# Optimization experiments

Hardware: AMD Instinct MI355X
Metric: run time of the kernel (lower is better)

## Reference

```python
import math
import jax, jax.numpy as jnp
from jax import lax
import numpy as np

WH, WW = 5, 9          # window_size
EH, EW = 3, 5          # expand_size = ((ws+1)//2)
NHEAD = 4
D = 512
PK, PS = 4, 4          # pool kernel / stride


def _valid_ind_rolled():
    m = np.ones((4, WH, WW), dtype=np.float32)
    m[0, :WH - EH, :WW - EW] = 0  # tl
    m[1, :WH - EH, EW:] = 0       # tr
    m[2, EH:, :WW - EW] = 0       # bl
    m[3, EH:, EW:] = 0            # br
    return np.nonzero(m.reshape(-1))[0]

VALID_IND = jnp.asarray(_valid_ind_rolled())  # (148,)


def _forward(x, masks, Wq, bq, Wk, bk, Wv, bv, Wp, bp, pool_w, pool_b):
    b, t, h, w, c = x.shape
    hd = c // NHEAD
    n_wh, n_ww = h // WH, w // WW
    n_win = n_wh * n_ww
    S = WH * WW  # tokens per window per frame (45)

    q = x @ Wq + bq
    k = x @ Wk + bk
    v = x @ Wv + bv

    def wp(a):  # window partition -> (b, n_win, nhead, t, S, hd)
        a = a.reshape(b, t, n_wh, WH, n_ww, WW, NHEAD, hd)
        a = a.transpose(0, 2, 4, 6, 1, 3, 5, 7)
        return a.reshape(b, n_win, NHEAD, t, S, hd)

    win_q, win_k, win_v = wp(q), wp(k), wp(v)

    # rolled (shifted) windows, gathered by the static valid-index buffer
    shifts = ((-EH, -EW), (-EH, EW), (EH, -EW), (EH, EW))
    roll_k = jnp.concatenate([wp(jnp.roll(k, s, axis=(2, 3))) for s in shifts], axis=4)[:, :, :, :, VALID_IND]
    roll_v = jnp.concatenate([wp(jnp.roll(v, s, axis=(2, 3))) for s in shifts], axis=4)[:, :, :, :, VALID_IND]

    # pooled global tokens via depthwise conv (kernel 4, stride 4)
    px = lax.conv_general_dilated(
        x.reshape(b * t, h, w, c), pool_w, (PS, PS), 'VALID',
        dimension_numbers=('NHWC', 'HWIO', 'NHWC'), feature_group_count=c) + pool_b
    ph, pw = px.shape[1], px.shape[2]
    P = ph * pw
    px = px.reshape(b, t, P, c)

    def pool_tok(a):  # (b,t,P,c) -> (b,1,nhead,t,P,hd)
        return a.reshape(b, t, P, NHEAD, hd).transpose(0, 3, 1, 2, 4)[:, None]

    pk = jnp.broadcast_to(pool_tok(px @ Wk + bk), (b, n_win, NHEAD, t, P, hd))
    pv = jnp.broadcast_to(pool_tok(px @ Wv + bv), (b, n_win, NHEAD, t, P, hd))

    win_k_full = jnp.concatenate([win_k, roll_k, pk], axis=4)  # (b,n_win,nh,t,K,hd)
    win_v_full = jnp.concatenate([win_v, roll_v, pv], axis=4)
    K = win_k_full.shape[4]

    # window-level mask: max-pool per window per frame, summed over frames, >0
    wmask = masks[..., 0].reshape(b, t, n_wh, WH, n_ww, WW).max(axis=(3, 5))
    wmask = wmask.reshape(b, t, n_win).sum(axis=1) > 0  # (b, n_win)

    scale = 1.0 / math.sqrt(hd)

    # dense spatiotemporal attention (used for masked windows)
    qd = win_q.reshape(b, n_win, NHEAD, t * S, hd)
    kd = win_k_full.reshape(b, n_win, NHEAD, t * K, hd)
    vd = win_v_full.reshape(b, n_win, NHEAD, t * K, hd)
    att_d = jax.nn.softmax(jnp.einsum('bnhqd,bnhkd->bnhqk', qd, kd) * scale, axis=-1)
    y_d = jnp.einsum('bnhqk,bnhkd->bnhqd', att_d, vd).reshape(b, n_win, NHEAD, t, S, hd)

    # per-frame local window attention (used for unmasked windows; keys = first S = window tokens)
    att_l = jax.nn.softmax(jnp.einsum('bnhtqd,bnhtkd->bnhtqk', win_q, win_k) * scale, axis=-1)
    y_l = jnp.einsum('bnhtqk,bnhtkd->bnhtqd', att_l, win_v)

    out = jnp.where(wmask[:, :, None, None, None, None], y_d, y_l)
    out = out.reshape(b, n_wh, n_ww, NHEAD, t, WH, WW, hd)
    out = out.transpose(0, 4, 1, 5, 2, 6, 3, 7).reshape(b, t, h, w, c)
    return out @ Wp + bp


def setup_inputs() -> dict:
    key = jax.random.key(0)
    ks = jax.random.split(key, 8)
    b, t, h, w = 1, 6, 40, 72
    x = jax.random.normal(ks[0], (b, t, h, w, D), dtype=jnp.float32)
    wm = (jax.random.uniform(ks[1], (b, t, h // WH, w // WW)) < 0.3).astype(jnp.float32)
    masks = jnp.repeat(jnp.repeat(wm, WH, axis=2), WW, axis=3)[..., None]
    s = 0.02

    def lin(kk):
        k1, k2 = jax.random.split(kk)
        return (jax.random.normal(k1, (D, D), jnp.float32) * s,
                jax.random.normal(k2, (D,), jnp.float32) * s)

    Wq, bq = lin(ks[2])
    Wk, bk = lin(ks[3])
    Wv, bv = lin(ks[4])
    Wp, bp = lin(ks[5])
    pool_w = jax.random.normal(ks[6], (PK, PK, 1, D), jnp.float32) * s
    pool_b = jax.random.normal(ks[7], (D,), jnp.float32) * s
    return {'x': x, 'masks': masks, 'Wq': Wq, 'bq': bq, 'Wk': Wk, 'bk': bk,
            'Wv': Wv, 'bv': bv, 'Wp': Wp, 'bp': bp, 'pool_w': pool_w, 'pool_b': pool_b}


def reference(x, masks, Wq, bq, Wk, bk, Wv, bv, Wp, bp, pool_w, pool_b):
    return _forward(x, masks, Wq, bq, Wk, bk, Wv, bv, Wp, bp, pool_w, pool_b)
```

## Files before the change

kernel.cpp:

```cpp
#include <hip/hip_runtime.h>

typedef unsigned short u16;
typedef unsigned int u32;
typedef __bf16 bf16x8 __attribute__((ext_vector_type(8)));
typedef float f32x4 __attribute__((ext_vector_type(4)));

#define TT 6
#define NTOK (6*40*72)
#define NPOOL 1080
#define MALL (NTOK + NPOOL)
#define KTOT 373
#define NKEYS (TT*KTOT)
#define NCH2 35
#define SCALE 0.08838834764831845f
#define K_EXP2 0.12751743f

__device__ __forceinline__ float bf2f(u16 u){ u32 x = ((u32)u) << 16; return __builtin_bit_cast(float, x); }
__device__ __forceinline__ u16 f2bf(float f){ return __builtin_bit_cast(u16, (__bf16)f); }

__device__ __forceinline__ void gload16(const u16* g, u16* l){
  __builtin_amdgcn_global_load_lds(
      (const __attribute__((address_space(1))) void*)g,
      (__attribute__((address_space(3))) void*)l, 16, 0, 0);
}

__global__ __launch_bounds__(256) void convert_x(const float* __restrict__ src, u16* __restrict__ dst, int n4)
{
  int i = blockIdx.x * 256 + threadIdx.x;
  if (i >= n4) return;
  float4 v = *(const float4*)(src + (size_t)i * 4);
  u16 o[4] = {f2bf(v.x), f2bf(v.y), f2bf(v.z), f2bf(v.w)};
  *(uint2*)(dst + (size_t)i * 4) = *(const uint2*)o;
}

__global__ __launch_bounds__(256) void transpose_w(
    const float* __restrict__ w0, const float* __restrict__ w1,
    const float* __restrict__ w2, const float* __restrict__ w3, u16* __restrict__ out)
{
  __shared__ float tile[64][65];
  int m = blockIdx.z;
  const float* src = m == 0 ? w0 : (m == 1 ? w1 : (m == 2 ? w2 : w3));
  int kb = blockIdx.x * 64, nb = blockIdx.y * 64;
  int tid = threadIdx.x;
  int tx = tid & 63, ty = tid >> 6;
#pragma unroll
  for (int i = 0; i < 16; i++)
    tile[ty + 4*i][tx] = src[(size_t)(kb + ty + 4*i) * 512 + nb + tx];
  __syncthreads();
#pragma unroll
  for (int i = 0; i < 16; i++)
    out[m * 262144 + (size_t)(nb + ty + 4*i) * 512 + kb + tx] = f2bf(tile[tx][ty + 4*i]);
}

__global__ __launch_bounds__(256) void gemm_bias(
    const u16* __restrict__ A, const u16* __restrict__ wt,
    const float* __restrict__ b0, const float* __restrict__ b1, const float* __restrict__ b2,
    u16* __restrict__ c0, u16* __restrict__ c1, u16* __restrict__ c2, float* __restrict__ cf,
    int wo0, int wo1, int wo2, int M)
{
  __shared__ __align__(16) u16 sA[128*32];
  __shared__ __align__(16) u16 sB[128*32];
  int z = blockIdx.z;
  const u16* Bt = wt + (size_t)(z == 0 ? wo0 : (z == 1 ? wo1 : wo2)) * 262144;
  const float* bias = z == 0 ? b0 : (z == 1 ? b1 : b2);
  u16* Cout = z == 0 ? c0 : (z == 1 ? c1 : c2);
  int mbase = blockIdx.x * 128, nbase = blockIdx.y * 128;
  int tid = threadIdx.x, lane = tid & 63, wave = tid >> 6;
  int wm = (wave >> 1) * 64, wn = (wave & 1) * 64;
  int quad = lane >> 4, tr = lane & 15;
  int lrow = lane >> 2;
  int seg  = (lane & 3) ^ (lrow & 3);

  const u16* gA[2]; const u16* gB[2];
#pragma unroll
  for (int r = 0; r < 2; r++){
    gA[r] = A  + (size_t)(mbase + wave*32 + r*16 + lrow) * 512 + seg*8;
    gB[r] = Bt + (size_t)(nbase + wave*32 + r*16 + lrow) * 512 + seg*8;
  }
  u16* lA[2]; u16* lB[2];
#pragma unroll
  for (int r = 0; r < 2; r++){
    lA[r] = &sA[(wave*32 + r*16) * 32];
    lB[r] = &sB[(wave*32 + r*16) * 32];
  }

  f32x4 acc[4][4];
#pragma unroll
  for (int i = 0; i < 4; i++)
#pragma unroll
    for (int j = 0; j < 4; j++){ acc[i][j][0]=0.f; acc[i][j][1]=0.f; acc[i][j][2]=0.f; acc[i][j][3]=0.f; }

  int rcol = (quad ^ (tr & 3)) * 8;

  for (int k0 = 0; k0 < 512; k0 += 32){
    if (k0) __syncthreads();
#pragma unroll
    for (int r = 0; r < 2; r++){
      gload16(gA[r] + k0, lA[r]);
      gload16(gB[r] + k0, lB[r]);
    }
    __syncthreads();
    bf16x8 a[4], b[4];
#pragma unroll
    for (int i = 0; i < 4; i++) a[i] = *(const bf16x8*)(&sA[(wm + i*16 + tr)*32 + rcol]);
#pragma unroll
    for (int j = 0; j < 4; j++) b[j] = *(const bf16x8*)(&sB[(wn + j*16 + tr)*32 + rcol]);
#pragma unroll
    for (int i = 0; i < 4; i++)
#pragma unroll
      for (int j = 0; j < 4; j++)
        acc[i][j] = __builtin_amdgcn_mfma_f32_16x16x32_bf16(a[i], b[j], acc[i][j], 0, 0, 0);
  }

#pragma unroll
  for (int j = 0; j < 4; j++){
    int col = nbase + wn + j*16 + tr;
    float bv = bias[col];
#pragma unroll
    for (int i = 0; i < 4; i++)
#pragma unroll
      for (int r2 = 0; r2 < 4; r2++){
        int row = mbase + wm + i*16 + quad*4 + r2;
        if (row < M){
          float val = acc[i][j][r2] + bv;
          if (cf) cf[(size_t)row * 512 + col] = val;
          else    Cout[(size_t)row * 512 + col] = f2bf(val);
        }
      }
  }
}

__global__ __launch_bounds__(256) void pool_conv(
    const float* __restrict__ x, const float* __restrict__ pw,
    const float* __restrict__ pb, u16* __restrict__ px)
{
  int idx = blockIdx.x * 256 + threadIdx.x;
  int c = idx & 511, n = idx >> 9;
  int f = n / 180, rp = n % 180, ph = rp / 18, pwc = rp % 18;
  float acc = pb[c];
#pragma unroll
  for (int i = 0; i < 4; i++)
#pragma unroll
    for (int j = 0; j < 4; j++){
      int hh = ph*4 + i, ww = pwc*4 + j;
      acc += x[((size_t)((f*40 + hh)*72 + ww)) * 512 + c] * pw[(i*4 + j)*512 + c];
    }
  px[idx] = f2bf(acc);
}

__global__ __launch_bounds__(256) void build_idx(
    const float* __restrict__ masks, int* __restrict__ wmask, int* __restrict__ idxTab)
{
  __shared__ int sVI[148];
  __shared__ int sFlag;
  int win = blockIdx.x, wi = win >> 3, wj = win & 7;
  int tid = threadIdx.x;
  if (tid == 0){
    sFlag = 0;
    int cnt = 0;
    for (int e = 0; e < 180; e++){
      int s = e / 45, pos = e % 45, pr = pos / 9, pc = pos % 9;
      bool inval = (s == 0 && pr < 2 && pc < 4) || (s == 1 && pr < 2 && pc >= 5) ||
                   (s == 2 && pr >= 3 && pc < 4) || (s == 3 && pr >= 3 && pc >= 5);
      if (!inval) sVI[cnt++] = e;
    }
  }
  __syncthreads();
  if (tid < 270){
    int f = tid / 45, p = tid - (tid / 45) * 45;
    int hh = wi*5 + p/9, ww = wj*9 + p%9;
    if (masks[(f*40 + hh)*72 + ww] > 0.f) atomicOr(&sFlag, 1);
  }
  __syncthreads();
  if (tid == 0) wmask[win] = sFlag;

  for (int i = tid; i < NKEYS; i += 256){
    int f = i / KTOT, slot = i - f * KTOT;
    int idx;
    if (slot < 45){
      int hh = wi*5 + slot/9, ww = wj*9 + slot%9;
      idx = ((f*40 + hh)*72 + ww) * 1024;
    } else if (slot < 193){
      int e = sVI[slot - 45];
      int s2 = e / 45, pos = e - s2*45, pr = pos/9, pc = pos - pr*9;
      int hh = wi*5 + pr + ((s2 < 2) ? 3 : -3);
      int ww = wj*9 + pc + ((s2 & 1) ? -5 : 5);
      if (hh < 0) hh += 40; else if (hh >= 40) hh -= 40;
      if (ww < 0) ww += 72; else if (ww >= 72) ww -= 72;
      idx = ((f*40 + hh)*72 + ww) * 1024;
    } else {
      idx = ~((f*180 + (slot - 193)) * 1024);
    }
    idxTab[win * 2240 + i] = idx;
  }
}

__global__ __launch_bounds__(512) void attn_dense(
    const u16* __restrict__ qb, const u16* __restrict__ kb, const u16* __restrict__ vb,
    const u16* __restrict__ pkb, const u16* __restrict__ pvb,
    const int* __restrict__ wmaskp, const int* __restrict__ idxTab,
    u16* __restrict__ yb)
{
  __shared__ __align__(16) u16 sK[64][136];
  __shared__ __align__(16) u16 sVt[128][72];
  __shared__ __align__(16) u32 sPw[288][36];
  __shared__ int sIdx[2240];
  __shared__ float sDenX[32];

  int win = blockIdx.x, head = blockIdx.y;
  if (!wmaskp[win]) return;
  int wi = win >> 3, wj = win & 7;
  int tid = threadIdx.x, lane = tid & 63, wave = tid >> 6;
  int quad = lane >> 4, tr = lane & 15;

  if (tid < 32) sDenX[tid] = 0.f;
  {
    const int* g = idxTab + win * 2240;
    for (int i = tid; i < NKEYS; i += 512) sIdx[i] = g[i];
  }

  int mts[3] = {2*wave, 2*wave + 1, 16 + (wave >> 2)};
  bf16x8 qf[3][4];
#pragma unroll
  for (int im = 0; im < 3; im++){
    int row = mts[im]*16 + tr;
    int f = row / 48, r = row - f*48;
    bool vld = r < 45;
    int hh = wi*5 + r/9, ww = wj*9 + r%9;
    const u16* qp = qb + ((size_t)((f*40 + hh)*72 + ww))*512 + head*128;
#pragma unroll
    for (int kt = 0; kt < 4; kt++){
      uint4 v = make_uint4(0,0,0,0);
      if (vld) v = *(const uint4*)(qp + kt*32 + quad*8);
      qf[im][kt] = __builtin_bit_cast(bf16x8, v);
    }
  }

  f32x4 accv[2][8], accx[2];
#pragma unroll
  for (int m = 0; m < 2; m++)
#pragma unroll
    for (int nt = 0; nt < 8; nt++){ accv[m][nt][0]=0.f; accv[m][nt][1]=0.f; accv[m][nt][2]=0.f; accv[m][nt][3]=0.f; }
  accx[0][0]=0.f; accx[0][1]=0.f; accx[0][2]=0.f; accx[0][3]=0.f;
  accx[1][0]=0.f; accx[1][1]=0.f; accx[1][2]=0.f; accx[1][3]=0.f;
  float dacc[2] = {0.f, 0.f};
  float daccx = 0.f;

  __syncthreads();

  int upair = tid & 31, dgv = tid >> 5;
  const char* kb2  = (const char*)kb  + head*256 + (tid & 15)*16;
  const char* pkb2 = (const char*)pkb + head*256 + (tid & 15)*16;
  const char* vb2  = (const char*)vb  + head*256 + dgv*16;
  const char* pvb2 = (const char*)pvb + head*256 + dgv*16;

  uint4 pfk[2], pfv[2];
  auto pref = [&](int ch){
#pragma unroll
    for (int r = 0; r < 2; r++){ pfk[r] = make_uint4(0,0,0,0); pfv[r] = make_uint4(0,0,0,0); }
    if (ch < NCH2){
      int base = ch * 64;
#pragma unroll
      for (int r = 0; r < 2; r++){
        int jg = base + (tid >> 4) + 32*r;
        if (jg < NKEYS){
          int off = sIdx[jg];
          pfk[r] = *(const uint4*)(off >= 0 ? kb2 + off : pkb2 + ~off);
        }
      }
#pragma unroll
      for (int r = 0; r < 2; r++){
        int jg = base + 2*upair + r;
        if (jg < NKEYS){
          int off = sIdx[jg];
          pfv[r] = *(const uint4*)(off >= 0 ? vb2 + off : pvb2 + ~off);
        }
      }
    }
  };
  pref(0);

  for (int ch = 0; ch < NCH2; ch++){
    __syncthreads();
#pragma unroll
    for (int r = 0; r < 2; r++)
      *(uint4*)(&sK[(tid >> 4) + 32*r][(tid & 15)*8]) = pfk[r];
    {
      u32 va[4] = {pfv[0].x, pfv[0].y, pfv[0].z, pfv[0].w};
      u32 vbp[4] = {pfv[1].x, pfv[1].y, pfv[1].z, pfv[1].w};
#pragma unroll
      for (int jj = 0; jj < 8; jj++){
        u32 lo = (va[jj >> 1] >> (16*(jj & 1))) & 0xffffu;
        u32 hi = (vbp[jj >> 1] >> (16*(jj & 1))) & 0xffffu;
        ((u32*)&sVt[dgv*8 + jj][0])[upair] = lo | (hi << 16);
      }
    }
    __syncthreads();
    pref(ch + 1);

#pragma unroll
    for (int nt = 0; nt < 4; nt++){
      bf16x8 bk[4];
#pragma unroll
      for (int kt = 0; kt < 4; kt++) bk[kt] = *(const bf16x8*)(&sK[nt*16 + tr][kt*32 + quad*8]);
      int colb = ch*64 + nt*16 + quad*4;
#pragma unroll
      for (int m = 0; m < 2; m++){
        f32x4 s = {0.f, 0.f, 0.f, 0.f};
#pragma unroll
        for (int kt = 0; kt < 4; kt++) s = __builtin_amdgcn_mfma_f32_16x16x32_bf16(bk[kt], qf[m][kt], s, 0, 0, 0);
        float p[4];
#pragma unroll
        for (int r2 = 0; r2 < 4; r2++){
          p[r2] = (colb + r2 < NKEYS) ? __builtin_amdgcn_exp2f(s[r2] * K_EXP2) : 0.f;
          dacc[m] += p[r2];
        }
        uint2 w;
        w.x = (u32)f2bf(p[0]) | ((u32)f2bf(p[1]) << 16);
        w.y = (u32)f2bf(p[2]) | ((u32)f2bf(p[3]) << 16);
        *(uint2*)(&sPw[(2*wave + m)*16 + tr][nt*8 + quad*2]) = w;
      }
      if (nt == (wave & 3)){
        f32x4 s = {0.f, 0.f, 0.f, 0.f};
#pragma unroll
        for (int kt = 0; kt < 4; kt++) s = __builtin_amdgcn_mfma_f32_16x16x32_bf16(bk[kt], qf[2][kt], s, 0, 0, 0);
        float p[4];
#pragma unroll
        for (int r2 = 0; r2 < 4; r2++){
          p[r2] = (colb + r2 < NKEYS) ? __builtin_amdgcn_exp2f(s[r2] * K_EXP2) : 0.f;
          daccx += p[r2];
        }
        uint2 w;
        w.x = (u32)f2bf(p[0]) | ((u32)f2bf(p[1]) << 16);
        w.y = (u32)f2bf(p[2]) | ((u32)f2bf(p[3]) << 16);
        *(uint2*)(&sPw[(16 + (wave >> 2))*16 + tr][nt*8 + quad*2]) = w;
      }
    }
    __syncthreads();

#pragma unroll
    for (int kt2 = 0; kt2 < 2; kt2++){
      bf16x8 a0 = *(const bf16x8*)(&sPw[(2*wave)*16 + tr][kt2*16 + quad*4]);
      bf16x8 a1 = *(const bf16x8*)(&sPw[(2*wave + 1)*16 + tr][kt2*16 + quad*4]);
      bf16x8 ax = *(const bf16x8*)(&sPw[(16 + (wave >> 2))*16 + tr][kt2*16 + quad*4]);
#pragma unroll
      for (int nt = 0; nt < 8; nt++){
        bf16x8 bv = *(const bf16x8*)(&sVt[nt*16 + tr][kt2*32 + quad*8]);
        accv[0][nt] = __builtin_amdgcn_mfma_f32_16x16x32_bf16(a0, bv, accv[0][nt], 0, 0, 0);
        accv[1][nt] = __builtin_amdgcn_mfma_f32_16x16x32_bf16(a1, bv, accv[1][nt], 0, 0, 0);
      }
      int he0 = (wave & 3)*2;
      bf16x8 bx0 = *(const bf16x8*)(&sVt[he0*16 + tr][kt2*32 + quad*8]);
      bf16x8 bx1 = *(const bf16x8*)(&sVt[(he0+1)*16 + tr][kt2*32 + quad*8]);
      accx[0] = __builtin_amdgcn_mfma_f32_16x16x32_bf16(ax, bx0, accx[0], 0, 0, 0);
      accx[1] = __builtin_amdgcn_mfma_f32_16x16x32_bf16(ax, bx1, accx[1], 0, 0, 0);
    }
  }

  float dred[2];
#pragma unroll
  for (int m = 0; m < 2; m++){
    float d = dacc[m];
    d += __shfl_xor(d, 16, 64); d += __shfl_xor(d, 32, 64);
    dred[m] = d;
  }
  {
    float d = daccx;
    d += __shfl_xor(d, 16, 64); d += __shfl_xor(d, 32, 64);
    if (lane < 16) atomicAdd(&sDenX[(wave >> 2)*16 + lane], d);
  }
  __syncthreads();

#pragma unroll
  for (int m = 0; m < 2; m++){
#pragma unroll
    for (int r2 = 0; r2 < 4; r2++){
      float dinvv = 1.f / __shfl(dred[m], quad*4 + r2, 64);
      int row = (2*wave + m)*16 + quad*4 + r2;
      int f = row / 48, r = row - f*48;
      if (r < 45){
        int hh = wi*5 + r/9, ww = wj*9 + r%9;
        size_t base = ((size_t)((f*40 + hh)*72 + ww))*512 + head*128;
#pragma unroll
        for (int nt = 0; nt < 8; nt++)
          yb[base + nt*16 + tr] = f2bf(accv[m][nt][r2] * dinvv);
      }
    }
  }
  {
    int e = 16 + (wave >> 2), he0 = (wave & 3)*2;
#pragma unroll
    for (int r2 = 0; r2 < 4; r2++){
      int row = e*16 + quad*4 + r2;
      int f = row / 48, r = row - f*48;
      if (r < 45){
        float dinvv = 1.f / sDenX[(e - 16)*16 + quad*4 + r2];
        int hh = wi*5 + r/9, ww = wj*9 + r%9;
        size_t base = ((size_t)((f*40 + hh)*72 + ww))*512 + head*128;
        yb[base + he0*16 + tr]       = f2bf(accx[0][r2] * dinvv);
        yb[base + (he0 + 1)*16 + tr] = f2bf(accx[1][r2] * dinvv);
      }
    }
  }
}

__device__ __forceinline__ const u16* key_src_local(int slot, int qf, int wi, int wj, int head,
    const u16* __restrict__ tokbuf)
{
  int hh = wi*5 + slot/9, ww = wj*9 + slot%9;
  return tokbuf + ((size_t)((qf*40 + hh)*72 + ww)) * 512 + head * 128;
}

__global__ __launch_bounds__(256) void attn_local(
    const u16* __restrict__ qb, const u16* __restrict__ kb, const u16* __restrict__ vb,
    const int* __restrict__ wmaskp, u16* __restrict__ yb)
{
  __shared__ __align__(16) u16 sQ[48][136];
  __shared__ __align__(16) u16 sK[64][136];
  __shared__ __align__(16) u16 sVt[128][72];
  __shared__ __align__(16) u16 sP[48][72];
  __shared__ float sDen[48];

  int win = blockIdx.x, head = blockIdx.y, qf = blockIdx.z;
  if (wmaskp[win]) return;
  int wi = win >> 3, wj = win & 7;
  int tid = threadIdx.x, lane = tid & 63, wave = tid >> 6;
  int quad = lane >> 4, tr = lane & 15;

  if (tid < 48) sDen[tid] = 0.f;

#pragma unroll
  for (int r = 0; r < 3; r++){
    int u = tid + 256 * r;
    int row = u >> 4, dg = u & 15;
    uint4 val = make_uint4(0,0,0,0);
    if (row < 45){
      int hh = wi*5 + row/9, ww = wj*9 + row%9;
      val = *(const uint4*)(qb + ((size_t)((qf*40 + hh)*72 + ww)) * 512 + head*128 + dg*8);
    }
    *(uint4*)(&sQ[row][dg * 8]) = val;
  }

  const int nkeys = 45;
  f32x4 acc[3][2];
#pragma unroll
  for (int a = 0; a < 3; a++)
#pragma unroll
    for (int b = 0; b < 2; b++){ acc[a][b][0]=0.f; acc[a][b][1]=0.f; acc[a][b][2]=0.f; acc[a][b][3]=0.f; }

#pragma unroll
  for (int r = 0; r < 4; r++){
    int u = tid + 256 * r;
    int key = u >> 4, dg = u & 15;
    uint4 val = make_uint4(0,0,0,0);
    if (key < nkeys) val = *(const uint4*)(key_src_local(key, qf, wi, wj, head, kb) + dg * 8);
    *(uint4*)(&sK[key][dg * 8]) = val;
  }
#pragma unroll
  for (int r = 0; r < 4; r++){
    int u = tid + 256 * r;
    int key = u & 63, dg = u >> 6;
    uint4 val = make_uint4(0,0,0,0);
    if (key < nkeys) val = *(const uint4*)(key_src_local(key, qf, wi, wj, head, vb) + dg * 8);
    u32 vv[4] = {val.x, val.y, val.z, val.w};
#pragma unroll
    for (int q2 = 0; q2 < 4; q2++){
      sVt[dg*8 + q2*2][key]     = (u16)(vv[q2] & 0xffff);
      sVt[dg*8 + q2*2 + 1][key] = (u16)(vv[q2] >> 16);
    }
  }
  __syncthreads();

#pragma unroll
  for (int mt = 0; mt < 3; mt++){
    f32x4 sacc = {0.f, 0.f, 0.f, 0.f};
#pragma unroll
    for (int kt = 0; kt < 4; kt++){
      bf16x8 a = *(const bf16x8*)(&sQ[mt*16 + tr][kt*32 + quad*8]);
      bf16x8 b = *(const bf16x8*)(&sK[wave*16 + tr][kt*32 + quad*8]);
      sacc = __builtin_amdgcn_mfma_f32_16x16x32_bf16(a, b, sacc, 0, 0, 0);
    }
    int colg = wave * 16 + tr;
    float pr4[4];
#pragma unroll
    for (int r2 = 0; r2 < 4; r2++){
      float p = (colg < nkeys) ? __builtin_amdgcn_exp2f(sacc[r2] * K_EXP2) : 0.f;
      sP[mt*16 + quad*4 + r2][wave*16 + tr] = f2bf(p);
      pr4[r2] = p;
    }
#pragma unroll
    for (int r2 = 0; r2 < 4; r2++){
      float ps = pr4[r2];
      ps += __shfl_xor(ps, 1, 64);
      ps += __shfl_xor(ps, 2, 64);
      ps += __shfl_xor(ps, 4, 64);
      ps += __shfl_xor(ps, 8, 64);
      if (tr == 0) atomicAdd(&sDen[mt*16 + quad*4 + r2], ps);
    }
  }
  __syncthreads();

#pragma unroll
  for (int mt = 0; mt < 3; mt++)
#pragma unroll
    for (int nt = 0; nt < 2; nt++)
#pragma unroll
      for (int kt = 0; kt < 2; kt++){
        bf16x8 a = *(const bf16x8*)(&sP[mt*16 + tr][kt*32 + quad*8]);
        bf16x8 b = *(const bf16x8*)(&sVt[wave*32 + nt*16 + tr][kt*32 + quad*8]);
        acc[mt][nt] = __builtin_amdgcn_mfma_f32_16x16x32_bf16(a, b, acc[mt][nt], 0, 0, 0);
      }
  __syncthreads();

#pragma unroll
  for (int mt = 0; mt < 3; mt++)
#pragma unroll
    for (int r2 = 0; r2 < 4; r2++){
      int row = mt*16 + quad*4 + r2;
      if (row < 45){
        float dinv = 1.0f / sDen[row];
        int hh = wi*5 + row/9, ww = wj*9 + row%9;
        size_t base = ((size_t)((qf*40 + hh)*72 + ww)) * 512 + head * 128;
#pragma unroll
        for (int nt = 0; nt < 2; nt++){
          int col = wave*32 + nt*16 + tr;
          yb[base + col] = f2bf(acc[mt][nt][r2] * dinv);
        }
      }
    }
}

extern "C" void kernel_launch(void* const* d_in, const int* in_sizes, int n_in,
                              void* d_out, int out_size, void* d_ws, size_t ws_size,
                              hipStream_t stream)
{
  const float* x     = (const float*)d_in[0];
  const float* masks = (const float*)d_in[1];
  const float* Wq = (const float*)d_in[2];  const float* bq = (const float*)d_in[3];
  const float* Wk = (const float*)d_in[4];  const float* bk = (const float*)d_in[5];
  const float* Wv = (const float*)d_in[6];  const float* bv = (const float*)d_in[7];
  const float* Wp = (const float*)d_in[8];  const float* bp = (const float*)d_in[9];
  const float* pw = (const float*)d_in[10]; const float* pb = (const float*)d_in[11];
  float* out = (float*)d_out;

  char* ws = (char*)d_ws;
  size_t off = 0;
  auto alloc = [&](size_t bytes) -> char* {
    char* p = ws + off; off += (bytes + 255) & ~(size_t)255; return p;
  };
  u16* wt    = (u16*)alloc((size_t)4 * 512 * 512 * 2);
  u16* xbf   = (u16*)alloc((size_t)18432 * 512 * 2);
  u16* qbuf  = (u16*)alloc((size_t)18432 * 512 * 2);
  u16* kbuf  = (u16*)alloc((size_t)18432 * 512 * 2);
  u16* vbuf  = (u16*)alloc((size_t)18432 * 512 * 2);
  u16* ybuf  = (u16*)alloc((size_t)NTOK * 512 * 2);
  int* wmaskb = (int*)alloc(64 * 4);
  int* idxTabb = (int*)alloc((size_t)64 * 2240 * 4);

  u16* pkbuf = kbuf + (size_t)NTOK * 512;
  u16* pvbuf = vbuf + (size_t)NTOK * 512;

  convert_x<<<dim3((NTOK*512/4 + 255)/256), 256, 0, stream>>>(x, xbf, NTOK*512/4);
  pool_conv<<<dim3(2160), 256, 0, stream>>>(x, pw, pb, xbf + (size_t)NTOK * 512);
  transpose_w<<<dim3(8, 8, 4), 256, 0, stream>>>(Wq, Wk, Wv, Wp, wt);
  gemm_bias<<<dim3(144, 4, 3), 256, 0, stream>>>(xbf, wt, bq, bk, bv, qbuf, kbuf, vbuf, nullptr, 0, 1, 2, MALL);
  build_idx<<<dim3(64), 256, 0, stream>>>(masks, wmaskb, idxTabb);
  attn_dense<<<dim3(64, 4), 512, 0, stream>>>(qbuf, kbuf, vbuf, pkbuf, pvbuf, wmaskb, idxTabb, ybuf);
  attn_local<<<dim3(64, 4, 6), 256, 0, stream>>>(qbuf, kbuf, vbuf, wmaskb, ybuf);
  gemm_bias<<<dim3(135, 4, 1), 256, 0, stream>>>(ybuf, wt, bp, bp, bp, nullptr, nullptr, nullptr, out, 3, 3, 3, NTOK);
}
```

Before: 357.3 us.

## Fuse preprocessing kernels and merge dense/local attention into one launch

Combines x conversion, pooled conv, weight transpose and index building into one kernel dispatched by block range. Merges the dense-window and local-window attention kernels into a single launch that branches on the window mask, with local windows processing the six frames in three iterations using two half-block groups. This removes several kernel launches and lets the two attention paths overlap on the GPU, at the cost of fewer blocks for local windows and a larger shared-memory footprint per block.

```diff
diff --git a/kernel.cpp b/kernel.cpp
--- a/kernel.cpp
+++ b/kernel.cpp
@@ -24,32 +24,91 @@
       (__attribute__((address_space(3))) void*)l, 16, 0, 0);
 }
 
-__global__ __launch_bounds__(256) void convert_x(const float* __restrict__ src, u16* __restrict__ dst, int n4)
+__global__ __launch_bounds__(256) void prep_all(
+    const float* __restrict__ x, const float* __restrict__ masks,
+    const float* __restrict__ w0, const float* __restrict__ w1,
+    const float* __restrict__ w2, const float* __restrict__ w3,
+    const float* __restrict__ pw, const float* __restrict__ pb,
+    u16* __restrict__ xbf, u16* __restrict__ wt,
+    int* __restrict__ wmask, int* __restrict__ idxTab)
 {
-  int i = blockIdx.x * 256 + threadIdx.x;
-  if (i >= n4) return;
-  float4 v = *(const float4*)(src + (size_t)i * 4);
-  u16 o[4] = {f2bf(v.x), f2bf(v.y), f2bf(v.z), f2bf(v.w)};
-  *(uint2*)(dst + (size_t)i * 4) = *(const uint2*)o;
-}
-
-__global__ __launch_bounds__(256) void transpose_w(
-    const float* __restrict__ w0, const float* __restrict__ w1,
-    const float* __restrict__ w2, const float* __restrict__ w3, u16* __restrict__ out)
-{
-  __shared__ float tile[64][65];
-  int m = blockIdx.z;
-  const float* src = m == 0 ? w0 : (m == 1 ? w1 : (m == 2 ? w2 : w3));
-  int kb = blockIdx.x * 64, nb = blockIdx.y * 64;
-  int tid = threadIdx.x;
-  int tx = tid & 63, ty = tid >> 6;
-#pragma unroll
-  for (int i = 0; i < 16; i++)
-    tile[ty + 4*i][tx] = src[(size_t)(kb + ty + 4*i) * 512 + nb + tx];
-  __syncthreads();
-#pragma unroll
-  for (int i = 0; i < 16; i++)
-    out[m * 262144 + (size_t)(nb + ty + 4*i) * 512 + kb + tx] = f2bf(tile[tx][ty + 4*i]);
+  __shared__ __align__(16) float tile[64][65];
+  int b = blockIdx.x, tid = threadIdx.x;
+
+  if (b < 8640){
+    int i = b * 256 + tid;
+    float4 v = *(const float4*)(x + (size_t)i * 4);
+    u16 o[4] = {f2bf(v.x), f2bf(v.y), f2bf(v.z), f2bf(v.w)};
+    *(uint2*)(xbf + (size_t)i * 4) = *(const uint2*)o;
+  } else if (b < 10800){
+    int idx = (b - 8640) * 256 + tid;
+    int c = idx & 511, n = idx >> 9;
+    int f = n / 180, rp = n % 180, ph = rp / 18, pwc = rp % 18;
+    float acc = pb[c];
+#pragma unroll
+    for (int i = 0; i < 4; i++)
+#pragma unroll
+      for (int j = 0; j < 4; j++){
+        int hh = ph*4 + i, ww = pwc*4 + j;
+        acc += x[((size_t)((f*40 + hh)*72 + ww)) * 512 + c] * pw[(i*4 + j)*512 + c];
+      }
+    xbf[(size_t)NTOK * 512 + idx] = f2bf(acc);
+  } else if (b < 11056){
+    int idx = b - 10800;
+    int m = idx >> 6, r = idx & 63;
+    int kb = (r >> 3) * 64, nb = (r & 7) * 64;
+    const float* src = m == 0 ? w0 : (m == 1 ? w1 : (m == 2 ? w2 : w3));
+    int tx = tid & 63, ty = tid >> 6;
+#pragma unroll
+    for (int i = 0; i < 16; i++)
+      tile[ty + 4*i][tx] = src[(size_t)(kb + ty + 4*i) * 512 + nb + tx];
+    __syncthreads();
+#pragma unroll
+    for (int i = 0; i < 16; i++)
+      wt[m * 262144 + (size_t)(nb + ty + 4*i) * 512 + kb + tx] = f2bf(tile[tx][ty + 4*i]);
+  } else {
+    int* sVI = (int*)&tile[0][0];
+    int* sFlag = sVI + 160;
+    int win = b - 11056, wi = win >> 3, wj = win & 7;
+    if (tid == 0){
+      sFlag[0] = 0;
+      int cnt = 0;
+      for (int e = 0; e < 180; e++){
+        int s = e / 45, pos = e % 45, pr = pos / 9, pc = pos % 9;
+        bool inval = (s == 0 && pr < 2 && pc < 4) || (s == 1 && pr < 2 && pc >= 5) ||
+                     (s == 2 && pr >= 3 && pc < 4) || (s == 3 && pr >= 3 && pc >= 5);
+        if (!inval) sVI[cnt++] = e;
+      }
+    }
+    __syncthreads();
+    if (tid < 270){
+      int f = tid / 45, p = tid - (tid / 45) * 45;
+      int hh = wi*5 + p/9, ww = wj*9 + p%9;
+      if (masks[(f*40 + hh)*72 + ww] > 0.f) atomicOr(sFlag, 1);
+    }
+    __syncthreads();
+    if (tid == 0) wmask[win] = sFlag[0];
+
+    for (int i = tid; i < NKEYS; i += 256){
+      int f = i / KTOT, slot = i - f * KTOT;
+      int idx;
+      if (slot < 45){
+        int hh = wi*5 + slot/9, ww = wj*9 + slot%9;
+        idx = ((f*40 + hh)*72 + ww) * 1024;
+      } else if (slot < 193){
+        int e = sVI[slot - 45];
+        int s2 = e / 45, pos = e - s2*45, pr = pos/9, pc = pos - pr*9;
+        int hh = wi*5 + pr + ((s2 < 2) ? 3 : -3);
+        int ww = wj*9 + pc + ((s2 & 1) ? -5 : 5);
+        if (hh < 0) hh += 40; else if (hh >= 40) hh -= 40;
+        if (ww < 0) ww += 72; else if (ww >= 72) ww -= 72;
+        idx = ((f*40 + hh)*72 + ww) * 1024;
+      } else {
+        idx = ~((f*180 + (slot - 193)) * 1024);
+      }
+      idxTab[win * 2240 + i] = idx;
+    }
+  }
 }
 
 __global__ __launch_bounds__(256) void gemm_bias(
@@ -130,280 +189,6 @@
   }
 }
 
-__global__ __launch_bounds__(256) void pool_conv(
-    const float* __restrict__ x, const float* __restrict__ pw,
-    const float* __restrict__ pb, u16* __restrict__ px)
-{
-  int idx = blockIdx.x * 256 + threadIdx.x;
-  int c = idx & 511, n = idx >> 9;
-  int f = n / 180, rp = n % 180, ph = rp / 18, pwc = rp % 18;
-  float acc = pb[c];
-#pragma unroll
-  for (int i = 0; i < 4; i++)
-#pragma unroll
-    for (int j = 0; j < 4; j++){
-      int hh = ph*4 + i, ww = pwc*4 + j;
-      acc += x[((size_t)((f*40 + hh)*72 + ww)) * 512 + c] * pw[(i*4 + j)*512 + c];
-    }
-  px[idx] = f2bf(acc);
-}
-
-__global__ __launch_bounds__(256) void build_idx(
-    const float* __restrict__ masks, int* __restrict__ wmask, int* __restrict__ idxTab)
-{
-  __shared__ int sVI[148];
-  __shared__ int sFlag;
-  int win = blockIdx.x, wi = win >> 3, wj = win & 7;
-  int tid = threadIdx.x;
-  if (tid == 0){
-    sFlag = 0;
-    int cnt = 0;
-    for (int e = 0; e < 180; e++){
-      int s = e / 45, pos = e % 45, pr = pos / 9, pc = pos % 9;
-      bool inval = (s == 0 && pr < 2 && pc < 4) || (s == 1 && pr < 2 && pc >= 5) ||
-                   (s == 2 && pr >= 3 && pc < 4) || (s == 3 && pr >= 3 && pc >= 5);
-      if (!inval) sVI[cnt++] = e;
-    }
-  }
-  __syncthreads();
-  if (tid < 270){
-    int f = tid / 45, p = tid - (tid / 45) * 45;
-    int hh = wi*5 + p/9, ww = wj*9 + p%9;
-    if (masks[(f*40 + hh)*72 + ww] > 0.f) atomicOr(&sFlag, 1);
-  }
-  __syncthreads();
-  if (tid == 0) wmask[win] = sFlag;
-
-  for (int i = tid; i < NKEYS; i += 256){
-    int f = i / KTOT, slot = i - f * KTOT;
-    int idx;
-    if (slot < 45){
-      int hh = wi*5 + slot/9, ww = wj*9 + slot%9;
-      idx = ((f*40 + hh)*72 + ww) * 1024;
-    } else if (slot < 193){
-      int e = sVI[slot - 45];
-      int s2 = e / 45, pos = e - s2*45, pr = pos/9, pc = pos - pr*9;
-      int hh = wi*5 + pr + ((s2 < 2) ? 3 : -3);
-      int ww = wj*9 + pc + ((s2 & 1) ? -5 : 5);
-      if (hh < 0) hh += 40; else if (hh >= 40) hh -= 40;
-      if (ww < 0) ww += 72; else if (ww >= 72) ww -= 72;
-      idx = ((f*40 + hh)*72 + ww) * 1024;
-    } else {
-      idx = ~((f*180 + (slot - 193)) * 1024);
-    }
-    idxTab[win * 2240 + i] = idx;
-  }
-}
-
-__global__ __launch_bounds__(512) void attn_dense(
-    const u16* __restrict__ qb, const u16* __restrict__ kb, const u16* __restrict__ vb,
-    const u16* __restrict__ pkb, const u16* __restrict__ pvb,
-    const int* __restrict__ wmaskp, const int* __restrict__ idxTab,
-    u16* __restrict__ yb)
-{
-  __shared__ __align__(16) u16 sK[64][136];
-  __shared__ __align__(16) u16 sVt[128][72];
-  __shared__ __align__(16) u32 sPw[288][36];
-  __shared__ int sIdx[2240];
-  __shared__ float sDenX[32];
-
-  int win = blockIdx.x, head = blockIdx.y;
-  if (!wmaskp[win]) return;
-  int wi = win >> 3, wj = win & 7;
-  int tid = threadIdx.x, lane = tid & 63, wave = tid >> 6;
-  int quad = lane >> 4, tr = lane & 15;
-
-  if (tid < 32) sDenX[tid] = 0.f;
-  {
-    const int* g = idxTab + win * 2240;
-    for (int i = tid; i < NKEYS; i += 512) sIdx[i] = g[i];
-  }
-
-  int mts[3] = {2*wave, 2*wave + 1, 16 + (wave >> 2)};
-  bf16x8 qf[3][4];
-#pragma unroll
-  for (int im = 0; im < 3; im++){
-    int row = mts[im]*16 + tr;
-    int f = row / 48, r = row - f*48;
-    bool vld = r < 45;
-    int hh = wi*5 + r/9, ww = wj*9 + r%9;
-    const u16* qp = qb + ((size_t)((f*40 + hh)*72 + ww))*512 + head*128;
-#pragma unroll
-    for (int kt = 0; kt < 4; kt++){
-      uint4 v = make_uint4(0,0,0,0);
-      if (vld) v = *(const uint4*)(qp + kt*32 + quad*8);
-      qf[im][kt] = __builtin_bit_cast(bf16x8, v);
-    }
-  }
-
-  f32x4 accv[2][8], accx[2];
-#pragma unroll
-  for (int m = 0; m < 2; m++)
-#pragma unroll
-    for (int nt = 0; nt < 8; nt++){ accv[m][nt][0]=0.f; accv[m][nt][1]=0.f; accv[m][nt][2]=0.f; accv[m][nt][3]=0.f; }
-  accx[0][0]=0.f; accx[0][1]=0.f; accx[0][2]=0.f; accx[0][3]=0.f;
-  accx[1][0]=0.f; accx[1][1]=0.f; accx[1][2]=0.f; accx[1][3]=0.f;
-  float dacc[2] = {0.f, 0.f};
-  float daccx = 0.f;
-
-  __syncthreads();
-
-  int upair = tid & 31, dgv = tid >> 5;
-  const char* kb2  = (const char*)kb  + head*256 + (tid & 15)*16;
-  const char* pkb2 = (const char*)pkb + head*256 + (tid & 15)*16;
-  const char* vb2  = (const char*)vb  + head*256 + dgv*16;
-  const char* pvb2 = (const char*)pvb + head*256 + dgv*16;
-
-  uint4 pfk[2], pfv[2];
-  auto pref = [&](int ch){
-#pragma unroll
-    for (int r = 0; r < 2; r++){ pfk[r] = make_uint4(0,0,0,0); pfv[r] = make_uint4(0,0,0,0); }
-    if (ch < NCH2){
-      int base = ch * 64;
-#pragma unroll
-      for (int r = 0; r < 2; r++){
-        int jg = base + (tid >> 4) + 32*r;
-        if (jg < NKEYS){
-          int off = sIdx[jg];
-          pfk[r] = *(const uint4*)(off >= 0 ? kb2 + off : pkb2 + ~off);
-        }
-      }
-#pragma unroll
-      for (int r = 0; r < 2; r++){
-        int jg = base + 2*upair + r;
-        if (jg < NKEYS){
-          int off = sIdx[jg];
-          pfv[r] = *(const uint4*)(off >= 0 ? vb2 + off : pvb2 + ~off);
-        }
-      }
-    }
-  };
-  pref(0);
-
-  for (int ch = 0; ch < NCH2; ch++){
-    __syncthreads();
-#pragma unroll
-    for (int r = 0; r < 2; r++)
-      *(uint4*)(&sK[(tid >> 4) + 32*r][(tid & 15)*8]) = pfk[r];
-    {
-      u32 va[4] = {pfv[0].x, pfv[0].y, pfv[0].z, pfv[0].w};
-      u32 vbp[4] = {pfv[1].x, pfv[1].y, pfv[1].z, pfv[1].w};
-#pragma unroll
-      for (int jj = 0; jj < 8; jj++){
-        u32 lo = (va[jj >> 1] >> (16*(jj & 1))) & 0xffffu;
-        u32 hi = (vbp[jj >> 1] >> (16*(jj & 1))) & 0xffffu;
-        ((u32*)&sVt[dgv*8 + jj][0])[upair] = lo | (hi << 16);
-      }
-    }
-    __syncthreads();
-    pref(ch + 1);
-
-#pragma unroll
-    for (int nt = 0; nt < 4; nt++){
-      bf16x8 bk[4];
-#pragma unroll
-      for (int kt = 0; kt < 4; kt++) bk[kt] = *(const bf16x8*)(&sK[nt*16 + tr][kt*32 + quad*8]);
-      int colb = ch*64 + nt*16 + quad*4;
-#pragma unroll
-      for (int m = 0; m < 2; m++){
-        f32x4 s = {0.f, 0.f, 0.f, 0.f};
-#pragma unroll
-        for (int kt = 0; kt < 4; kt++) s = __builtin_amdgcn_mfma_f32_16x16x32_bf16(bk[kt], qf[m][kt], s, 0, 0, 0);
-        float p[4];
-#pragma unroll
-        for (int r2 = 0; r2 < 4; r2++){
-          p[r2] = (colb + r2 < NKEYS) ? __builtin_amdgcn_exp2f(s[r2] * K_EXP2) : 0.f;
-          dacc[m] += p[r2];
-        }
-        uint2 w;
-        w.x = (u32)f2bf(p[0]) | ((u32)f2bf(p[1]) << 16);
-        w.y = (u32)f2bf(p[2]) | ((u32)f2bf(p[3]) << 16);
-        *(uint2*)(&sPw[(2*wave + m)*16 + tr][nt*8 + quad*2]) = w;
-      }
-      if (nt == (wave & 3)){
-        f32x4 s = {0.f, 0.f, 0.f, 0.f};
-#pragma unroll
-        for (int kt = 0; kt < 4; kt++) s = __builtin_amdgcn_mfma_f32_16x16x32_bf16(bk[kt], qf[2][kt], s, 0, 0, 0);
-        float p[4];
-#pragma unroll
-        for (int r2 = 0; r2 < 4; r2++){
-          p[r2] = (colb + r2 < NKEYS) ? __builtin_amdgcn_exp2f(s[r2] * K_EXP2) : 0.f;
-          daccx += p[r2];
-        }
-        uint2 w;
-        w.x = (u32)f2bf(p[0]) | ((u32)f2bf(p[1]) << 16);
-        w.y = (u32)f2bf(p[2]) | ((u32)f2bf(p[3]) << 16);
-        *(uint2*)(&sPw[(16 + (wave >> 2))*16 + tr][nt*8 + quad*2]) = w;
-      }
-    }
-    __syncthreads();
-
-#pragma unroll
-    for (int kt2 = 0; kt2 < 2; kt2++){
-      bf16x8 a0 = *(const bf16x8*)(&sPw[(2*wave)*16 + tr][kt2*16 + quad*4]);
-      bf16x8 a1 = *(const bf16x8*)(&sPw[(2*wave + 1)*16 + tr][kt2*16 + quad*4]);
-      bf16x8 ax = *(const bf16x8*)(&sPw[(16 + (wave >> 2))*16 + tr][kt2*16 + quad*4]);
-#pragma unroll
-      for (int nt = 0; nt < 8; nt++){
-        bf16x8 bv = *(const bf16x8*)(&sVt[nt*16 + tr][kt2*32 + quad*8]);
-        accv[0][nt] = __builtin_amdgcn_mfma_f32_16x16x32_bf16(a0, bv, accv[0][nt], 0, 0, 0);
-        accv[1][nt] = __builtin_amdgcn_mfma_f32_16x16x32_bf16(a1, bv, accv[1][nt], 0, 0, 0);
-      }
-      int he0 = (wave & 3)*2;
-      bf16x8 bx0 = *(const bf16x8*)(&sVt[he0*16 + tr][kt2*32 + quad*8]);
-      bf16x8 bx1 = *(const bf16x8*)(&sVt[(he0+1)*16 + tr][kt2*32 + quad*8]);
-      accx[0] = __builtin_amdgcn_mfma_f32_16x16x32_bf16(ax, bx0, accx[0], 0, 0, 0);
-      accx[1] = __builtin_amdgcn_mfma_f32_16x16x32_bf16(ax, bx1, accx[1], 0, 0, 0);
-    }
-  }
-
-  float dred[2];
-#pragma unroll
-  for (int m = 0; m < 2; m++){
-    float d = dacc[m];
-    d += __shfl_xor(d, 16, 64); d += __shfl_xor(d, 32, 64);
-    dred[m] = d;
-  }
-  {
-    float d = daccx;
-    d += __shfl_xor(d, 16, 64); d += __shfl_xor(d, 32, 64);
-    if (lane < 16) atomicAdd(&sDenX[(wave >> 2)*16 + lane], d);
-  }
-  __syncthreads();
-
-#pragma unroll
-  for (int m = 0; m < 2; m++){
-#pragma unroll
-    for (int r2 = 0; r2 < 4; r2++){
-      float dinvv = 1.f / __shfl(dred[m], quad*4 + r2, 64);
-      int row = (2*wave + m)*16 + quad*4 + r2;
-      int f = row / 48, r = row - f*48;
-      if (r < 45){
-        int hh = wi*5 + r/9, ww = wj*9 + r%9;
-        size_t base = ((size_t)((f*40 + hh)*72 + ww))*512 + head*128;
-#pragma unroll
-        for (int nt = 0; nt < 8; nt++)
-          yb[base + nt*16 + tr] = f2bf(accv[m][nt][r2] * dinvv);
-      }
-    }
-  }
-  {
-    int e = 16 + (wave >> 2), he0 = (wave & 3)*2;
-#pragma unroll
-    for (int r2 = 0; r2 < 4; r2++){
-      int row = e*16 + quad*4 + r2;
-      int f = row / 48, r = row - f*48;
-      if (r < 45){
-        float dinvv = 1.f / sDenX[(e - 16)*16 + quad*4 + r2];
-        int hh = wi*5 + r/9, ww = wj*9 + r%9;
-        size_t base = ((size_t)((f*40 + hh)*72 + ww))*512 + head*128;
-        yb[base + he0*16 + tr]       = f2bf(accx[0][r2] * dinvv);
-        yb[base + (he0 + 1)*16 + tr] = f2bf(accx[1][r2] * dinvv);
-      }
-    }
-  }
-}
-
 __device__ __forceinline__ const u16* key_src_local(int slot, int qf, int wi, int wj, int head,
     const u16* __restrict__ tokbuf)
 {
@@ -411,123 +196,329 @@
   return tokbuf + ((size_t)((qf*40 + hh)*72 + ww)) * 512 + head * 128;
 }
 
-__global__ __launch_bounds__(256) void attn_local(
+__global__ __launch_bounds__(512) void attn(
     const u16* __restrict__ qb, const u16* __restrict__ kb, const u16* __restrict__ vb,
-    const int* __restrict__ wmaskp, u16* __restrict__ yb)
+    const u16* __restrict__ pkb, const u16* __restrict__ pvb,
+    const int* __restrict__ wmaskp, const int* __restrict__ idxTab,
+    u16* __restrict__ yb)
 {
-  __shared__ __align__(16) u16 sQ[48][136];
-  __shared__ __align__(16) u16 sK[64][136];
-  __shared__ __align__(16) u16 sVt[128][72];
-  __shared__ __align__(16) u16 sP[48][72];
-  __shared__ float sDen[48];
-
-  int win = blockIdx.x, head = blockIdx.y, qf = blockIdx.z;
-  if (wmaskp[win]) return;
+  __shared__ __align__(16) char smem[112000];
+  int win = blockIdx.x, head = blockIdx.y;
   int wi = win >> 3, wj = win & 7;
   int tid = threadIdx.x, lane = tid & 63, wave = tid >> 6;
   int quad = lane >> 4, tr = lane & 15;
 
-  if (tid < 48) sDen[tid] = 0.f;
-
-#pragma unroll
-  for (int r = 0; r < 3; r++){
-    int u = tid + 256 * r;
-    int row = u >> 4, dg = u & 15;
-    uint4 val = make_uint4(0,0,0,0);
-    if (row < 45){
-      int hh = wi*5 + row/9, ww = wj*9 + row%9;
-      val = *(const uint4*)(qb + ((size_t)((qf*40 + hh)*72 + ww)) * 512 + head*128 + dg*8);
-    }
-    *(uint4*)(&sQ[row][dg * 8]) = val;
+  if (wmaskp[win]){
+    u16 (*sK)[136] = (u16(*)[136])smem;
+    u16 (*sVt)[72] = (u16(*)[72])(smem + 17408);
+    u32 (*sPw)[36] = (u32(*)[36])(smem + 35840);
+    int*  sIdx     = (int*)(smem + 77312);
+    float* sDenX   = (float*)(smem + 86272);
+
+    if (tid < 32) sDenX[tid] = 0.f;
+    {
+      const int* g = idxTab + win * 2240;
+      for (int i = tid; i < NKEYS; i += 512) sIdx[i] = g[i];
+    }
+
+    int mts[3] = {2*wave, 2*wave + 1, 16 + (wave >> 2)};
+    bf16x8 qf[3][4];
+#pragma unroll
+    for (int im = 0; im < 3; im++){
+      int row = mts[im]*16 + tr;
+      int f = row / 48, r = row - f*48;
+      bool vld = r < 45;
+      int hh = wi*5 + r/9, ww = wj*9 + r%9;
+      const u16* qp = qb + ((size_t)((f*40 + hh)*72 + ww))*512 + head*128;
+#pragma unroll
+      for (int kt = 0; kt < 4; kt++){
+        uint4 v = make_uint4(0,0,0,0);
+        if (vld) v = *(const uint4*)(qp + kt*32 + quad*8);
+        qf[im][kt] = __builtin_bit_cast(bf16x8, v);
+      }
+    }
+
+    f32x4 accv[2][8], accx[2];
+#pragma unroll
+    for (int m = 0; m < 2; m++)
+#pragma unroll
+      for (int nt = 0; nt < 8; nt++){ accv[m][nt][0]=0.f; accv[m][nt][1]=0.f; accv[m][nt][2]=0.f; accv[m][nt][3]=0.f; }
+    accx[0][0]=0.f; accx[0][1]=0.f; accx[0][2]=0.f; accx[0][3]=0.f;
+    accx[1][0]=0.f; accx[1][1]=0.f; accx[1][2]=0.f; accx[1][3]=0.f;
+    float dacc[2] = {0.f, 0.f};
+    float daccx = 0.f;
+
+    __syncthreads();
+
+    int upair = tid & 31, dgv = tid >> 5;
+    const char* kb2  = (const char*)kb  + head*256 + (tid & 15)*16;
+    const char* pkb2 = (const char*)pkb + head*256 + (tid & 15)*16;
+    const char* vb2  = (const char*)vb  + head*256 + dgv*16;
+    const char* pvb2 = (const char*)pvb + head*256 + dgv*16;
+
+    uint4 pfk[2], pfv[2];
+    auto pref = [&](int ch){
+#pragma unroll
+      for (int r = 0; r < 2; r++){ pfk[r] = make_uint4(0,0,0,0); pfv[r] = make_uint4(0,0,0,0); }
+      if (ch < NCH2){
+        int base = ch * 64;
+#pragma unroll
+        for (int r = 0; r < 2; r++){
+          int jg = base + (tid >> 4) + 32*r;
+          if (jg < NKEYS){
+            int off = sIdx[jg];
+            pfk[r] = *(const uint4*)(off >= 0 ? kb2 + off : pkb2 + ~off);
+          }
+        }
+#pragma unroll
+        for (int r = 0; r < 2; r++){
+          int jg = base + 2*upair + r;
+          if (jg < NKEYS){
+            int off = sIdx[jg];
+            pfv[r] = *(const uint4*)(off >= 0 ? vb2 + off : pvb2 + ~off);
+          }
+        }
+      }
+    };
+    pref(0);
+
+    for (int ch = 0; ch < NCH2; ch++){
+      __syncthreads();
+#pragma unroll
+      for (int r = 0; r < 2; r++)
+        *(uint4*)(&sK[(tid >> 4) + 32*r][(tid & 15)*8]) = pfk[r];
+      {
+        u32 va[4] = {pfv[0].x, pfv[0].y, pfv[0].z, pfv[0].w};
+        u32 vbp[4] = {pfv[1].x, pfv[1].y, pfv[1].z, pfv[1].w};
+#pragma unroll
+        for (int jj = 0; jj < 8; jj++){
+          u32 lo = (va[jj >> 1] >> (16*(jj & 1))) & 0xffffu;
+          u32 hi = (vbp[jj >> 1] >> (16*(jj & 1))) & 0xffffu;
+          ((u32*)&sVt[dgv*8 + jj][0])[upair] = lo | (hi << 16);
+        }
+      }
+      __syncthreads();
+      pref(ch + 1);
+
+#pragma unroll
+      for (int nt = 0; nt < 4; nt++){
+        bf16x8 bk[4];
+#pragma unroll
+        for (int kt = 0; kt < 4; kt++) bk[kt] = *(const bf16x8*)(&sK[nt*16 + tr][kt*32 + quad*8]);
+        int colb = ch*64 + nt*16 + quad*4;
+#pragma unroll
+        for (int m = 0; m < 2; m++){
+          f32x4 s = {0.f, 0.f, 0.f, 0.f};
+#pragma unroll
+          for (int kt = 0; kt < 4; kt++) s = __builtin_amdgcn_mfma_f32_16x16x32_bf16(bk[kt], qf[m][kt], s, 0, 0, 0);
+          float p[4];
+#pragma unroll
+          for (int r2 = 0; r2 < 4; r2++){
+            p[r2] = (colb + r2 < NKEYS) ? __builtin_amdgcn_exp2f(s[r2] * K_EXP2) : 0.f;
+            dacc[m] += p[r2];
+          }
+          uint2 w;
+          w.x = (u32)f2bf(p[0]) | ((u32)f2bf(p[1]) << 16);
+          w.y = (u32)f2bf(p[2]) | ((u32)f2bf(p[3]) << 16);
+          *(uint2*)(&sPw[(2*wave + m)*16 + tr][nt*8 + quad*2]) = w;
+        }
+        if (nt == (wave & 3)){
+          f32x4 s = {0.f, 0.f, 0.f, 0.f};
+#pragma unroll
+          for (int kt = 0; kt < 4; kt++) s = __builtin_amdgcn_mfma_f32_16x16x32_bf16(bk[kt], qf[2][kt], s, 0, 0, 0);
+          float p[4];
+#pragma unroll
+          for (int r2 = 0; r2 < 4; r2++){
+            p[r2] = (colb + r2 < NKEYS) ? __builtin_amdgcn_exp2f(s[r2] * K_EXP2) : 0.f;
+            daccx += p[r2];
+          }
+          uint2 w;
+          w.x = (u32)f2bf(p[0]) | ((u32)f2bf(p[1]) << 16);
+          w.y = (u32)f2bf(p[2]) | ((u32)f2bf(p[3]) << 16);
+          *(uint2*)(&sPw[(16 + (wave >> 2))*16 + tr][nt*8 + quad*2]) = w;
+        }
+      }
+      __syncthreads();
+
+#pragma unroll
+      for (int kt2 = 0; kt2 < 2; kt2++){
+        bf16x8 a0 = *(const bf16x8*)(&sPw[(2*wave)*16 + tr][kt2*16 + quad*4]);
+        bf16x8 a1 = *(const bf16x8*)(&sPw[(2*wave + 1)*16 + tr][kt2*16 + quad*4]);
+        bf16x8 ax = *(const bf16x8*)(&sPw[(16 + (wave >> 2))*16 + tr][kt2*16 + quad*4]);
+#pragma unroll
+        for (int nt = 0; nt < 8; nt++){
+          bf16x8 bv = *(const bf16x8*)(&sVt[nt*16 + tr][kt2*32 + quad*8]);
+          accv[0][nt] = __builtin_amdgcn_mfma_f32_16x16x32_bf16(a0, bv, accv[0][nt], 0, 0, 0);
+          accv[1][nt] = __builtin_amdgcn_mfma_f32_16x16x32_bf16(a1, bv, accv[1][nt], 0, 0, 0);
+        }
+        int he0 = (wave & 3)*2;
+        bf16x8 bx0 = *(const bf16x8*)(&sVt[he0*16 + tr][kt2*32 + quad*8]);
+        bf16x8 bx1 = *(const bf16x8*)(&sVt[(he0+1)*16 + tr][kt2*32 + quad*8]);
+        accx[0] = __builtin_amdgcn_mfma_f32_16x16x32_bf16(ax, bx0, accx[0], 0, 0, 0);
+        accx[1] = __builtin_amdgcn_mfma_f32_16x16x32_bf16(ax, bx1, accx[1], 0, 0, 0);
+      }
+    }
+
+    float dred[2];
+#pragma unroll
+    for (int m = 0; m < 2; m++){
+      float d = dacc[m];
+      d += __shfl_xor(d, 16, 64); d += __shfl_xor(d, 32, 64);
+      dred[m] = d;
+    }
+    {
+      float d = daccx;
+      d += __shfl_xor(d, 16, 64); d += __shfl_xor(d, 32, 64);
+      if (lane < 16) atomicAdd(&sDenX[(wave >> 2)*16 + lane], d);
+    }
+    __syncthreads();
+
+#pragma unroll
+    for (int m = 0; m < 2; m++){
+#pragma unroll
+      for (int r2 = 0; r2 < 4; r2++){
+        float dinvv = 1.f / __shfl(dred[m], quad*4 + r2, 64);
+        int row = (2*wave + m)*16 + quad*4 + r2;
+        int f = row / 48, r = row - f*48;
+        if (r < 45){
+          int hh = wi*5 + r/9, ww = wj*9 + r%9;
+          size_t base = ((size_t)((f*40 + hh)*72 + ww))*512 + head*128;
+#pragma unroll
+          for (int nt = 0; nt < 8; nt++)
+            yb[base + nt*16 + tr] = f2bf(accv[m][nt][r2] * dinvv);
+        }
+      }
+    }
+    {
+      int e = 16 + (wave >> 2), he0 = (wave & 3)*2;
+#pragma unroll
+      for (int r2 = 0; r2 < 4; r2++){
+        int row = e*16 + quad*4 + r2;
+        int f = row / 48, r = row - f*48;
+        if (r < 45){
+          float dinvv = 1.f / sDenX[(e - 16)*16 + quad*4 + r2];
+          int hh = wi*5 + r/9, ww = wj*9 + r%9;
+          size_t base = ((size_t)((f*40 + hh)*72 + ww))*512 + head*128;
+          yb[base + he0*16 + tr]       = f2bf(accx[0][r2] * dinvv);
+          yb[base + (he0 + 1)*16 + tr] = f2bf(accx[1][r2] * dinvv);
+        }
+      }
+    }
+  } else {
+    int half = wave >> 2, lwave = wave & 3, ltid = tid & 255;
+    char* base = smem + half * 56000;
+    u16 (*sQ)[136]  = (u16(*)[136])base;
+    u16 (*sK)[136]  = (u16(*)[136])(base + 13056);
+    u16 (*sVt)[72]  = (u16(*)[72])(base + 30464);
+    u16 (*sP)[72]   = (u16(*)[72])(base + 48896);
+    float* sDen     = (float*)(base + 55808);
+    const int nkeys = 45;
+
+    for (int it = 0; it < 3; it++){
+      int qf = it*2 + half;
+      if (it) __syncthreads();
+      if (ltid < 48) sDen[ltid] = 0.f;
+
+#pragma unroll
+      for (int r = 0; r < 3; r++){
+        int u = ltid + 256 * r;
+        int row = u >> 4, dg = u & 15;
+        uint4 val = make_uint4(0,0,0,0);
+        if (row < 45){
+          int hh = wi*5 + row/9, ww = wj*9 + row%9;
+          val = *(const uint4*)(qb + ((size_t)((qf*40 + hh)*72 + ww)) * 512 + head*128 + dg*8);
+        }
+        *(uint4*)(&sQ[row][dg * 8]) = val;
+      }
+
+      f32x4 acc[3][2];
+#pragma unroll
+      for (int a = 0; a < 3; a++)
+#pragma unroll
+        for (int b2 = 0; b2 < 2; b2++){ acc[a][b2][0]=0.f; acc[a][b2][1]=0.f; acc[a][b2][2]=0.f; acc[a][b2][3]=0.f; }
+
+#pragma unroll
+      for (int r = 0; r < 4; r++){
+        int u = ltid + 256 * r;
+        int key = u >> 4, dg = u & 15;
+        uint4 val = make_uint4(0,0,0,0);
+        if (key < nkeys) val = *(const uint4*)(key_src_local(key, qf, wi, wj, head, kb) + dg * 8);
+        *(uint4*)(&sK[key][dg * 8]) = val;
+      }
+#pragma unroll
+      for (int r = 0; r < 4; r++){
+        int u = ltid + 256 * r;
+        int key = u & 63, dg = u >> 6;
+        uint4 val = make_uint4(0,0,0,0);
+        if (key < nkeys) val = *(const uint4*)(key_src_local(key, qf, wi, wj, head, vb) + dg * 8);
+        u32 vv[4] = {val.x, val.y, val.z, val.w};
+#pragma unroll
+        for (int q2 = 0; q2 < 4; q2++){
+          sVt[dg*8 + q2*2][key]     = (u16)(vv[q2] & 0xffff);
+          sVt[dg*8 + q2*2 + 1][key] = (u16)(vv[q2] >> 16);
+        }
+      }
+      __syncthreads();
+
+#pragma unroll
+      for (int mt = 0; mt < 3; mt++){
+        f32x4 sacc = {0.f, 0.f, 0.f, 0.f};
+#pragma unroll
+        for (int kt = 0; kt < 4; kt++){
+          bf16x8 a = *(const bf16x8*)(&sQ[mt*16 + tr][kt*32 + quad*8]);
+          bf16x8 b2 = *(const bf16x8*)(&sK[lwave*16 + tr][kt*32 + quad*8]);
+          sacc = __builtin_amdgcn_mfma_f32_16x16x32_bf16(a, b2, sacc, 0, 0, 0);
+        }
+        int colg = lwave * 16 + tr;
+        float pr4[4];
+#pragma unroll
+        for (int r2 = 0; r2 < 4; r2++){
+          float p = (colg < nkeys) ? __builtin_amdgcn_exp2f(sacc[r2] * K_EXP2) : 0.f;
+          sP[mt*16 + quad*4 + r2][lwave*16 + tr] = f2bf(p);
+          pr4[r2] = p;
+        }
+#pragma unroll
+        for (int r2 = 0; r2 < 4; r2++){
+          float ps = pr4[r2];
+          ps += __shfl_xor(ps, 1, 64);
+          ps += __shfl_xor(ps, 2, 64);
+          ps += __shfl_xor(ps, 4, 64);
+          ps += __shfl_xor(ps, 8, 64);
+          if (tr == 0) atomicAdd(&sDen[mt*16 + quad*4 + r2], ps);
+        }
+      }
+      __syncthreads();
+
+#pragma unroll
+      for (int mt = 0; mt < 3; mt++)
+#pragma unroll
+        for (int nt = 0; nt < 2; nt++)
+#pragma unroll
+          for (int kt = 0; kt < 2; kt++){
+            bf16x8 a = *(const bf16x8*)(&sP[mt*16 + tr][kt*32 + quad*8]);
+            bf16x8 b2 = *(const bf16x8*)(&sVt[lwave*32 + nt*16 + tr][kt*32 + quad*8]);
+            acc[mt][nt] = __builtin_amdgcn_mfma_f32_16x16x32_bf16(a, b2, acc[mt][nt], 0, 0, 0);
+          }
+      __syncthreads();
+
+#pragma unroll
+      for (int mt = 0; mt < 3; mt++)
+#pragma unroll
+        for (int r2 = 0; r2 < 4; r2++){
+          int row = mt*16 + quad*4 + r2;
+          if (row < 45){
+            float dinv = 1.0f / sDen[row];
+            int hh = wi*5 + row/9, ww = wj*9 + row%9;
+            size_t obase = ((size_t)((qf*40 + hh)*72 + ww)) * 512 + head * 128;
+#pragma unroll
+            for (int nt = 0; nt < 2; nt++){
+              int col = lwave*32 + nt*16 + tr;
+              yb[obase + col] = f2bf(acc[mt][nt][r2] * dinv);
+            }
+          }
+        }
+    }
   }
-
-  const int nkeys = 45;
-  f32x4 acc[3][2];
-#pragma unroll
-  for (int a = 0; a < 3; a++)
-#pragma unroll
-    for (int b = 0; b < 2; b++){ acc[a][b][0]=0.f; acc[a][b][1]=0.f; acc[a][b][2]=0.f; acc[a][b][3]=0.f; }
-
-#pragma unroll
-  for (int r = 0; r < 4; r++){
-    int u = tid + 256 * r;
-    int key = u >> 4, dg = u & 15;
-    uint4 val = make_uint4(0,0,0,0);
-    if (key < nkeys) val = *(const uint4*)(key_src_local(key, qf, wi, wj, head, kb) + dg * 8);
-    *(uint4*)(&sK[key][dg * 8]) = val;
-  }
-#pragma unroll
-  for (int r = 0; r < 4; r++){
-    int u = tid + 256 * r;
-    int key = u & 63, dg = u >> 6;
-    uint4 val = make_uint4(0,0,0,0);
-    if (key < nkeys) val = *(const uint4*)(key_src_local(key, qf, wi, wj, head, vb) + dg * 8);
-    u32 vv[4] = {val.x, val.y, val.z, val.w};
-#pragma unroll
-    for (int q2 = 0; q2 < 4; q2++){
-      sVt[dg*8 + q2*2][key]     = (u16)(vv[q2] & 0xffff);
-      sVt[dg*8 + q2*2 + 1][key] = (u16)(vv[q2] >> 16);
-    }
-  }
-  __syncthreads();
-
-#pragma unroll
-  for (int mt = 0; mt < 3; mt++){
-    f32x4 sacc = {0.f, 0.f, 0.f, 0.f};
-#pragma unroll
-    for (int kt = 0; kt < 4; kt++){
-      bf16x8 a = *(const bf16x8*)(&sQ[mt*16 + tr][kt*32 + quad*8]);
-      bf16x8 b = *(const bf16x8*)(&sK[wave*16 + tr][kt*32 + quad*8]);
-      sacc = __builtin_amdgcn_mfma_f32_16x16x32_bf16(a, b, sacc, 0, 0, 0);
-    }
-    int colg = wave * 16 + tr;
-    float pr4[4];
-#pragma unroll
-    for (int r2 = 0; r2 < 4; r2++){
-      float p = (colg < nkeys) ? __builtin_amdgcn_exp2f(sacc[r2] * K_EXP2) : 0.f;
-      sP[mt*16 + quad*4 + r2][wave*16 + tr] = f2bf(p);
-      pr4[r2] = p;
-    }
-#pragma unroll
-    for (int r2 = 0; r2 < 4; r2++){
-      float ps = pr4[r2];
-      ps += __shfl_xor(ps, 1, 64);
-      ps += __shfl_xor(ps, 2, 64);
-      ps += __shfl_xor(ps, 4, 64);
-      ps += __shfl_xor(ps, 8, 64);
-      if (tr == 0) atomicAdd(&sDen[mt*16 + quad*4 + r2], ps);
-    }
-  }
-  __syncthreads();
-
-#pragma unroll
-  for (int mt = 0; mt < 3; mt++)
-#pragma unroll
-    for (int nt = 0; nt < 2; nt++)
-#pragma unroll
-      for (int kt = 0; kt < 2; kt++){
-        bf16x8 a = *(const bf16x8*)(&sP[mt*16 + tr][kt*32 + quad*8]);
-        bf16x8 b = *(const bf16x8*)(&sVt[wave*32 + nt*16 + tr][kt*32 + quad*8]);
-        acc[mt][nt] = __builtin_amdgcn_mfma_f32_16x16x32_bf16(a, b, acc[mt][nt], 0, 0, 0);
-      }
-  __syncthreads();
-
-#pragma unroll
-  for (int mt = 0; mt < 3; mt++)
-#pragma unroll
-    for (int r2 = 0; r2 < 4; r2++){
-      int row = mt*16 + quad*4 + r2;
-      if (row < 45){
-        float dinv = 1.0f / sDen[row];
-        int hh = wi*5 + row/9, ww = wj*9 + row%9;
-        size_t base = ((size_t)((qf*40 + hh)*72 + ww)) * 512 + head * 128;
-#pragma unroll
-        for (int nt = 0; nt < 2; nt++){
-          int col = wave*32 + nt*16 + tr;
-          yb[base + col] = f2bf(acc[mt][nt][r2] * dinv);
-        }
-      }
-    }
 }
 
 extern "C" void kernel_launch(void* const* d_in, const int* in_sizes, int n_in,
@@ -560,12 +551,8 @@
   u16* pkbuf = kbuf + (size_t)NTOK * 512;
   u16* pvbuf = vbuf + (size_t)NTOK * 512;
 
-  convert_x<<<dim3((NTOK*512/4 + 255)/256), 256, 0, stream>>>(x, xbf, NTOK*512/4);
-  pool_conv<<<dim3(2160), 256, 0, stream>>>(x, pw, pb, xbf + (size_t)NTOK * 512);
-  transpose_w<<<dim3(8, 8, 4), 256, 0, stream>>>(Wq, Wk, Wv, Wp, wt);
+  prep_all<<<dim3(11120), 256, 0, stream>>>(x, masks, Wq, Wk, Wv, Wp, pw, pb, xbf, wt, wmaskb, idxTabb);
   gemm_bias<<<dim3(144, 4, 3), 256, 0, stream>>>(xbf, wt, bq, bk, bv, qbuf, kbuf, vbuf, nullptr, 0, 1, 2, MALL);
-  build_idx<<<dim3(64), 256, 0, stream>>>(masks, wmaskb, idxTabb);
-  attn_dense<<<dim3(64, 4), 512, 0, stream>>>(qbuf, kbuf, vbuf, pkbuf, pvbuf, wmaskb, idxTabb, ybuf);
-  attn_local<<<dim3(64, 4, 6), 256, 0, stream>>>(qbuf, kbuf, vbuf, wmaskb, ybuf);
+  attn<<<dim3(64, 4), 512, 0, stream>>>(qbuf, kbuf, vbuf, pkbuf, pvbuf, wmaskb, idxTabb, ybuf);
   gemm_bias<<<dim3(135, 4, 1), 256, 0, stream>>>(ybuf, wt, bp, bp, bp, nullptr, nullptr, nullptr, out, 3, 3, 3, NTOK);
 }
```

New measurement: 329.2 us. -7.8%, faster.
